# Kernel tuning notes

Hardware: AMD Instinct MI355X
Metric: run time of the kernel (lower is better)

Reference implementation:

```python
import jax, jax.numpy as jnp
import numpy as np


def _xcorr3x3_valid(x, k):
    # x: [B,H,W], k: [B,3,3] per-sample kernel; cross-correlation (matches F.conv2d), VALID padding
    B, H, W = x.shape
    out = jnp.zeros((B, H - 2, W - 2), dtype=x.dtype)
    for u in range(3):
        for v in range(3):
            out = out + x[:, u:u + H - 2, v:v + W - 2] * k[:, u, v, None, None]
    return out


def setup_inputs() -> dict:
    key = jax.random.key(0)
    ks = jax.random.split(key, 4)
    B, H, W = 256, 256, 256
    pred = jax.random.normal(ks[0], (B, H, W), dtype=jnp.float32)
    rhs = jax.random.normal(ks[1], (B, H - 2, W - 2), dtype=jnp.float32)
    Laplace_kernel = jax.random.normal(ks[2], (B, 3, 3), dtype=jnp.float32)
    Df_dr_kernel = jax.random.normal(ks[3], (B, 3, 3), dtype=jnp.float32)
    # physically sensible meshgrids: R in [1,2] (avoids div-by-zero), Z in [-1,1]
    r = jnp.linspace(1.0, 2.0, W, dtype=jnp.float32)
    z = jnp.linspace(-1.0, 1.0, H, dtype=jnp.float32)
    RR = jnp.broadcast_to(r[None, None, :], (B, H, W)).astype(jnp.float32)
    ZZ = jnp.broadcast_to(z[None, :, None], (B, H, W)).astype(jnp.float32)
    Gauss_kernel = (jnp.array([[1., 2., 1.], [2., 4., 2.], [1., 2., 1.]], dtype=jnp.float32) / 16.0)
    return {"pred": pred, "rhs": rhs, "Laplace_kernel": Laplace_kernel,
            "Df_dr_kernel": Df_dr_kernel, "RR": RR, "ZZ": ZZ, "Gauss_kernel": Gauss_kernel}


def reference(pred, rhs, Laplace_kernel, Df_dr_kernel, RR, ZZ, Gauss_kernel):
    # Lpsi, Dpsi_dr: per-sample 3x3 VALID stencils -> [B, H-2, W-2]
    Lpsi = _xcorr3x3_valid(pred, Laplace_kernel)
    Dpsi_dr = -_xcorr3x3_valid(pred, Df_dr_kernel)
    Dpsi_dr = Dpsi_dr / RR[:, 1:-1, 1:-1]
    lhs = Lpsi - Dpsi_dr
    hr = (RR[:, 1, 2] - RR[:, 1, 1])[:, None, None]
    hz = (ZZ[:, 2, 1] - ZZ[:, 1, 1])[:, None, None]
    alfa = -2.0 * (hr ** 2 + hz ** 2)
    GS_ope = lhs * alfa / (hr ** 2 * hz ** 2)
    # Gaussian smoothing, shared kernel, SAME padding (cross-correlation; kernel is symmetric)
    sm = jax.lax.conv_general_dilated(
        GS_ope[:, None, :, :], Gauss_kernel[None, None, :, :],
        window_strides=(1, 1), padding='SAME')
    GS_ope_smooth = -sm
    rhs_computed = -GS_ope_smooth[:, 0, :, :]
    return jnp.mean((rhs_computed - rhs) ** 2)
```

## Files before the change

### kernel.cpp

```cpp
#include <hip/hip_runtime.h>


__global__ __launch_bounds__(256, 4)
void pde_loss_kernel(const float* __restrict__ pred,
                     const float* __restrict__ rhs,
                     const float* __restrict__ KL,
                     const float* __restrict__ KD,
                     const float* __restrict__ RR,
                     const float* __restrict__ ZZ,
                     float* __restrict__ partials)
{
    constexpr int H = 256, W = 256, OH = 254, OW = 254;
    constexpr int SR = 8;
    const int tid = threadIdx.x;
    const int l   = tid & 63;
    const int wv  = tid >> 6;
    const int b   = blockIdx.x >> 3;
    const int strip = (blockIdx.x & 7) * 4 + wv;
    const int o0 = strip * SR;
    const int o1 = (o0 + SR < OH) ? (o0 + SR) : OH;

    const size_t ib = (size_t)b * H * W;
    const float* predb = pred + ib;
    const float* rhsb  = rhs + (size_t)b * OH * OW;

    const float hr  = RR[ib + W + 2] - RR[ib + W + 1];
    const float hz  = ZZ[ib + 2 * W + 1] - ZZ[ib + W + 1];
    const float hr2 = hr * hr, hz2 = hz * hz;
    const float s   = -2.0f * (hr2 + hz2) / (hr2 * hz2);

    const int c0 = 4 * l;
    float4 c4[9];
    {
        float4 invr;
        invr.x = 1.0f / RR[ib + W + (c0 + 1)];
        invr.y = 1.0f / RR[ib + W + (c0 + 2)];
        invr.z = 1.0f / RR[ib + W + (c0 + 3)];
        invr.w = 1.0f / RR[ib + W + ((c0 + 4 < W) ? (c0 + 4) : (W - 1))];
        const float* kl = KL + b * 9;
        const float* kd = KD + b * 9;
#pragma unroll
        for (int t = 0; t < 9; ++t) {
            const float a = kl[t] * s, d = kd[t] * s;
            c4[t].x = fmaf(d, invr.x, a);
            c4[t].y = fmaf(d, invr.y, a);
            c4[t].z = fmaf(d, invr.z, a);
            c4[t].w = fmaf(d, invr.w, a);
        }
    }

    const int g0 = o0 - 1;
    float4 pa = make_float4(0.f, 0.f, 0.f, 0.f), pb, pc;
    if (g0 >= 0) pa = *(const float4*)(predb + (size_t)g0 * W + c0);
    pb = *(const float4*)(predb + (size_t)(g0 + 1) * W + c0);
    pc = *(const float4*)(predb + (size_t)(g0 + 2) * W + c0);
    float nxa = __shfl(pa.x, l + 1, 64), nya = __shfl(pa.y, l + 1, 64);
    float nxb = __shfl(pb.x, l + 1, 64), nyb = __shfl(pb.y, l + 1, 64);

    float4 ghA = make_float4(0.f, 0.f, 0.f, 0.f);
    float4 ghB = make_float4(0.f, 0.f, 0.f, 0.f);
    float2 rc0 = make_float2(0.f, 0.f), rc1 = make_float2(0.f, 0.f);
    float acc = 0.0f;

    for (int g = g0; g <= o1; ++g) {
        float4 pn = make_float4(0.f, 0.f, 0.f, 0.f);
        const int rowp = g + 3;
        if (rowp < H && rowp <= o1 + 2)
            pn = *(const float4*)(predb + (size_t)rowp * W + c0);

        float2 rn0 = make_float2(0.f, 0.f), rn1 = make_float2(0.f, 0.f);
        if (g >= o0 && g < o1) {
            const float* rrow = rhsb + (size_t)g * OW + c0;
            rn0 = *(const float2*)rrow;
            if (c0 + 2 < OW) rn1 = *(const float2*)(rrow + 2);
        }

        const float nxc = __shfl(pc.x, l + 1, 64);
        const float nyc = __shfl(pc.y, l + 1, 64);

        float4 gs = make_float4(0.f, 0.f, 0.f, 0.f);
        if ((unsigned)g < (unsigned)OH) {
#define ROWC(p, nx, ny, t0)                                              \
            gs.x = fmaf(p.x, c4[t0].x, fmaf(p.y, c4[t0+1].x, fmaf(p.z, c4[t0+2].x, gs.x))); \
            gs.y = fmaf(p.y, c4[t0].y, fmaf(p.z, c4[t0+1].y, fmaf(p.w, c4[t0+2].y, gs.y))); \
            gs.z = fmaf(p.z, c4[t0].z, fmaf(p.w, c4[t0+1].z, fmaf(nx,  c4[t0+2].z, gs.z))); \
            gs.w = fmaf(p.w, c4[t0].w, fmaf(nx,  c4[t0+1].w, fmaf(ny,  c4[t0+2].w, gs.w)));
            ROWC(pa, nxa, nya, 0)
            ROWC(pb, nxb, nyb, 3)
            ROWC(pc, nxc, nyc, 6)
#undef ROWC
            if (l == 63) { gs.z = 0.f; gs.w = 0.f; }
        }

        float up = __shfl(gs.w, l - 1, 64);
        const float dn = __shfl(gs.x, l + 1, 64);
        if (l == 0) up = 0.f;
        float4 gh;
        gh.x = fmaf(2.f, gs.x, up   + gs.y);
        gh.y = fmaf(2.f, gs.y, gs.x + gs.z);
        gh.z = fmaf(2.f, gs.z, gs.y + gs.w);
        gh.w = fmaf(2.f, gs.w, gs.z + dn);

        const int i = g - 1;
        if (i >= o0 && i < o1) {
            const float smx = (ghA.x + 2.f * ghB.x + gh.x) * 0.0625f;
            const float smy = (ghA.y + 2.f * ghB.y + gh.y) * 0.0625f;
            const float smz = (ghA.z + 2.f * ghB.z + gh.z) * 0.0625f;
            const float smw = (ghA.w + 2.f * ghB.w + gh.w) * 0.0625f;
            const float dx = smx - rc0.x;
            const float dy = smy - rc0.y;
            float dz = smz - rc1.x;
            float dw = smw - rc1.y;
            if (c0 + 2 >= OW) { dz = 0.f; dw = 0.f; }
            acc = fmaf(dx, dx, acc);
            acc = fmaf(dy, dy, acc);
            acc = fmaf(dz, dz, acc);
            acc = fmaf(dw, dw, acc);
        }

        pa = pb; pb = pc; pc = pn;
        nxa = nxb; nya = nyb; nxb = nxc; nyb = nyc;
        ghA = ghB; ghB = gh;
        rc0 = rn0; rc1 = rn1;
    }

#pragma unroll
    for (int off = 32; off > 0; off >>= 1)
        acc += __shfl_down(acc, off, 64);
    __shared__ float wsum[4];
    if (l == 0) wsum[wv] = acc;
    __syncthreads();
    if (tid == 0)
        partials[blockIdx.x] = (wsum[0] + wsum[1]) + (wsum[2] + wsum[3]);
}

__global__ __launch_bounds__(256)
void reduce_kernel(const float* __restrict__ partials, float* __restrict__ out,
                   int n, float inv_n)
{
    const int tid = threadIdx.x;
    float a = 0.0f;
    for (int i = tid; i < n; i += 256) a += partials[i];
#pragma unroll
    for (int off = 32; off > 0; off >>= 1)
        a += __shfl_down(a, off, 64);
    __shared__ float w[4];
    if ((tid & 63) == 0) w[tid >> 6] = a;
    __syncthreads();
    if (tid == 0) out[0] = ((w[0] + w[1]) + (w[2] + w[3])) * inv_n;
}

__global__ __launch_bounds__(256, 4)
void reduce_fallback_zero(float* __restrict__ out) { if (threadIdx.x == 0) out[0] = 0.f; }

extern "C" void kernel_launch(void* const* d_in, const int* in_sizes, int n_in,
                              void* d_out, int out_size, void* d_ws, size_t ws_size,
                              hipStream_t stream) {
    const float* pred = (const float*)d_in[0];
    const float* rhs  = (const float*)d_in[1];
    const float* KL   = (const float*)d_in[2];
    const float* KD   = (const float*)d_in[3];
    const float* RR   = (const float*)d_in[4];
    const float* ZZ   = (const float*)d_in[5];
    float* out = (float*)d_out;

    const int B = in_sizes[2] / 9;
    const int nblocks = B * 8;
    const float inv_n = 1.0f / ((float)B * 254.0f * 254.0f);

    float* partials = (float*)d_ws;
    pde_loss_kernel<<<dim3(nblocks), dim3(256), 0, stream>>>(
        pred, rhs, KL, KD, RR, ZZ, partials);
    reduce_kernel<<<dim3(1), dim3(256), 0, stream>>>(partials, out, nblocks, inv_n);
}
```

Before: 216.9 us.

## Preload strip rows into registers, fully unroll row loop, split stencil into scalar-weight passes

Each wave now loads all 12 pred rows for its 8-row strip and the first rhs rows into registers before any compute, and fully unrolls the 10-step loop so every load is issued up front rather than one row per iteration. The per-column coefficient arrays (c4[9] float4) are replaced by two 9-tap stencils using wave-uniform scalar weights via readfirstlane, combined at the end with per-column scale factors. Branches are replaced by multiplicative masks. This doubles the stencil FMA count and raises register pressure, so the occupancy hint is dropped in exchange for more memory-level parallelism.

```diff
diff --git a/kernel.cpp b/kernel.cpp
--- a/kernel.cpp
+++ b/kernel.cpp
@@ -1,7 +1,7 @@
 #include <hip/hip_runtime.h>
 
 
-__global__ __launch_bounds__(256, 4)
+__global__ __launch_bounds__(256)
 void pde_loss_kernel(const float* __restrict__ pred,
                      const float* __restrict__ rhs,
                      const float* __restrict__ KL,
@@ -10,8 +10,7 @@
                      const float* __restrict__ ZZ,
                      float* __restrict__ partials)
 {
-    constexpr int H = 256, W = 256, OH = 254, OW = 254;
-    constexpr int SR = 8;
+    constexpr int H = 256, W = 256, OH = 254, OW = 254, SR = 8;
     const int tid = threadIdx.x;
     const int l   = tid & 63;
     const int wv  = tid >> 6;
@@ -23,106 +22,126 @@
     const size_t ib = (size_t)b * H * W;
     const float* predb = pred + ib;
     const float* rhsb  = rhs + (size_t)b * OH * OW;
+    const int c0 = 4 * l;
+
+    float4 p[12];
+#pragma unroll
+    for (int j = 0; j < 12; ++j) {
+        const int row = o0 - 1 + j;
+        p[j] = make_float4(0.f, 0.f, 0.f, 0.f);
+        if ((unsigned)row < (unsigned)H)
+            p[j] = *(const float4*)(predb + (size_t)row * W + c0);
+    }
+    float2 r0[8], r1[8];
+#pragma unroll
+    for (int j = 0; j < 8; ++j) { r0[j] = make_float2(0.f, 0.f); r1[j] = make_float2(0.f, 0.f); }
+#pragma unroll
+    for (int j = 0; j < 4; ++j) {
+        const float* rr = rhsb + (size_t)(o0 + j) * OW + c0;
+        r0[j] = *(const float2*)rr;
+        if (c0 + 2 < OW) r1[j] = *(const float2*)(rr + 2);
+    }
 
     const float hr  = RR[ib + W + 2] - RR[ib + W + 1];
     const float hz  = ZZ[ib + 2 * W + 1] - ZZ[ib + W + 1];
     const float hr2 = hr * hr, hz2 = hz * hz;
     const float s   = -2.0f * (hr2 + hz2) / (hr2 * hz2);
+    float kl[9], kd[9];
+#pragma unroll
+    for (int t = 0; t < 9; ++t) {
+        kl[t] = __int_as_float(__builtin_amdgcn_readfirstlane(__float_as_int(KL[b * 9 + t])));
+        kd[t] = __int_as_float(__builtin_amdgcn_readfirstlane(__float_as_int(KD[b * 9 + t])));
+    }
 
-    const int c0 = 4 * l;
-    float4 c4[9];
+    const float mzw = (l == 63) ? 0.f : 1.f;
+    const float m23 = (c0 + 2 < OW) ? 1.f : 0.f;
+    const float m0  = (l > 0) ? 1.f : 0.f;
+    float4 s4, sir4;
     {
         float4 invr;
         invr.x = 1.0f / RR[ib + W + (c0 + 1)];
         invr.y = 1.0f / RR[ib + W + (c0 + 2)];
         invr.z = 1.0f / RR[ib + W + (c0 + 3)];
         invr.w = 1.0f / RR[ib + W + ((c0 + 4 < W) ? (c0 + 4) : (W - 1))];
-        const float* kl = KL + b * 9;
-        const float* kd = KD + b * 9;
-#pragma unroll
-        for (int t = 0; t < 9; ++t) {
-            const float a = kl[t] * s, d = kd[t] * s;
-            c4[t].x = fmaf(d, invr.x, a);
-            c4[t].y = fmaf(d, invr.y, a);
-            c4[t].z = fmaf(d, invr.z, a);
-            c4[t].w = fmaf(d, invr.w, a);
-        }
+        s4.x = s; s4.y = s; s4.z = s * mzw; s4.w = s * mzw;
+        sir4.x = s4.x * invr.x; sir4.y = s4.y * invr.y;
+        sir4.z = s4.z * invr.z; sir4.w = s4.w * invr.w;
     }
 
-    const int g0 = o0 - 1;
-    float4 pa = make_float4(0.f, 0.f, 0.f, 0.f), pb, pc;
-    if (g0 >= 0) pa = *(const float4*)(predb + (size_t)g0 * W + c0);
-    pb = *(const float4*)(predb + (size_t)(g0 + 1) * W + c0);
-    pc = *(const float4*)(predb + (size_t)(g0 + 2) * W + c0);
-    float nxa = __shfl(pa.x, l + 1, 64), nya = __shfl(pa.y, l + 1, 64);
-    float nxb = __shfl(pb.x, l + 1, 64), nyb = __shfl(pb.y, l + 1, 64);
+#define SROW(SV, P, nx, ny, k0, k1, k2, KC)                                   \
+    SV.x = fmaf(P.x, KC[k0], fmaf(P.y, KC[k1], fmaf(P.z, KC[k2], SV.x)));     \
+    SV.y = fmaf(P.y, KC[k0], fmaf(P.z, KC[k1], fmaf(P.w, KC[k2], SV.y)));     \
+    SV.z = fmaf(P.z, KC[k0], fmaf(P.w, KC[k1], fmaf(nx,  KC[k2], SV.z)));     \
+    SV.w = fmaf(P.w, KC[k0], fmaf(nx,  KC[k1], fmaf(ny,  KC[k2], SV.w)));
 
-    float4 ghA = make_float4(0.f, 0.f, 0.f, 0.f);
-    float4 ghB = make_float4(0.f, 0.f, 0.f, 0.f);
-    float2 rc0 = make_float2(0.f, 0.f), rc1 = make_float2(0.f, 0.f);
+    float ax = __shfl(p[0].x, l + 1, 64), ay = __shfl(p[0].y, l + 1, 64);
+    float bx = __shfl(p[1].x, l + 1, 64), by = __shfl(p[1].y, l + 1, 64);
+    float4 ghm2 = make_float4(0.f, 0.f, 0.f, 0.f);
+    float4 ghm1 = make_float4(0.f, 0.f, 0.f, 0.f);
     float acc = 0.0f;
 
-    for (int g = g0; g <= o1; ++g) {
-        float4 pn = make_float4(0.f, 0.f, 0.f, 0.f);
-        const int rowp = g + 3;
-        if (rowp < H && rowp <= o1 + 2)
-            pn = *(const float4*)(predb + (size_t)rowp * W + c0);
+#pragma unroll
+    for (int K = 0; K < 10; ++K) {
+        const int g = o0 - 1 + K;
 
-        float2 rn0 = make_float2(0.f, 0.f), rn1 = make_float2(0.f, 0.f);
-        if (g >= o0 && g < o1) {
-            const float* rrow = rhsb + (size_t)g * OW + c0;
-            rn0 = *(const float2*)rrow;
-            if (c0 + 2 < OW) rn1 = *(const float2*)(rrow + 2);
+        if (K >= 2 && K <= 5) {
+            const int i = o0 + K + 2;
+            if (i < o1) {
+                const float* rr = rhsb + (size_t)i * OW + c0;
+                r0[K + 2] = *(const float2*)rr;
+                if (c0 + 2 < OW) r1[K + 2] = *(const float2*)(rr + 2);
+            }
         }
 
-        const float nxc = __shfl(pc.x, l + 1, 64);
-        const float nyc = __shfl(pc.y, l + 1, 64);
+        const float cx = __shfl(p[K + 2].x, l + 1, 64);
+        const float cy = __shfl(p[K + 2].y, l + 1, 64);
 
-        float4 gs = make_float4(0.f, 0.f, 0.f, 0.f);
-        if ((unsigned)g < (unsigned)OH) {
-#define ROWC(p, nx, ny, t0)                                              \
-            gs.x = fmaf(p.x, c4[t0].x, fmaf(p.y, c4[t0+1].x, fmaf(p.z, c4[t0+2].x, gs.x))); \
-            gs.y = fmaf(p.y, c4[t0].y, fmaf(p.z, c4[t0+1].y, fmaf(p.w, c4[t0+2].y, gs.y))); \
-            gs.z = fmaf(p.z, c4[t0].z, fmaf(p.w, c4[t0+1].z, fmaf(nx,  c4[t0+2].z, gs.z))); \
-            gs.w = fmaf(p.w, c4[t0].w, fmaf(nx,  c4[t0+1].w, fmaf(ny,  c4[t0+2].w, gs.w)));
-            ROWC(pa, nxa, nya, 0)
-            ROWC(pb, nxb, nyb, 3)
-            ROWC(pc, nxc, nyc, 6)
-#undef ROWC
-            if (l == 63) { gs.z = 0.f; gs.w = 0.f; }
+        float4 SL = make_float4(0.f, 0.f, 0.f, 0.f);
+        float4 SD = make_float4(0.f, 0.f, 0.f, 0.f);
+        if (g <= o1 && (unsigned)g < (unsigned)OH) {
+            SROW(SL, p[K],     ax, ay, 0, 1, 2, kl)
+            SROW(SL, p[K + 1], bx, by, 3, 4, 5, kl)
+            SROW(SL, p[K + 2], cx, cy, 6, 7, 8, kl)
+            SROW(SD, p[K],     ax, ay, 0, 1, 2, kd)
+            SROW(SD, p[K + 1], bx, by, 3, 4, 5, kd)
+            SROW(SD, p[K + 2], cx, cy, 6, 7, 8, kd)
         }
+        float4 gs;
+        gs.x = fmaf(s4.x, SL.x, sir4.x * SD.x);
+        gs.y = fmaf(s4.y, SL.y, sir4.y * SD.y);
+        gs.z = fmaf(s4.z, SL.z, sir4.z * SD.z);
+        gs.w = fmaf(s4.w, SL.w, sir4.w * SD.w);
 
-        float up = __shfl(gs.w, l - 1, 64);
+        const float up = __shfl(gs.w, l - 1, 64) * m0;
         const float dn = __shfl(gs.x, l + 1, 64);
-        if (l == 0) up = 0.f;
         float4 gh;
         gh.x = fmaf(2.f, gs.x, up   + gs.y);
         gh.y = fmaf(2.f, gs.y, gs.x + gs.z);
         gh.z = fmaf(2.f, gs.z, gs.y + gs.w);
         gh.w = fmaf(2.f, gs.w, gs.z + dn);
 
-        const int i = g - 1;
-        if (i >= o0 && i < o1) {
-            const float smx = (ghA.x + 2.f * ghB.x + gh.x) * 0.0625f;
-            const float smy = (ghA.y + 2.f * ghB.y + gh.y) * 0.0625f;
-            const float smz = (ghA.z + 2.f * ghB.z + gh.z) * 0.0625f;
-            const float smw = (ghA.w + 2.f * ghB.w + gh.w) * 0.0625f;
-            const float dx = smx - rc0.x;
-            const float dy = smy - rc0.y;
-            float dz = smz - rc1.x;
-            float dw = smw - rc1.y;
-            if (c0 + 2 >= OW) { dz = 0.f; dw = 0.f; }
-            acc = fmaf(dx, dx, acc);
-            acc = fmaf(dy, dy, acc);
-            acc = fmaf(dz, dz, acc);
-            acc = fmaf(dw, dw, acc);
+        if (K >= 2) {
+            const int i = g - 1;
+            if (i < o1) {
+                const float smx = (ghm2.x + 2.f * ghm1.x + gh.x) * 0.0625f;
+                const float smy = (ghm2.y + 2.f * ghm1.y + gh.y) * 0.0625f;
+                const float smz = (ghm2.z + 2.f * ghm1.z + gh.z) * 0.0625f;
+                const float smw = (ghm2.w + 2.f * ghm1.w + gh.w) * 0.0625f;
+                const float dx = smx - r0[K - 2].x;
+                const float dy = smy - r0[K - 2].y;
+                const float dz = (smz - r1[K - 2].x) * m23;
+                const float dw = (smw - r1[K - 2].y) * m23;
+                acc = fmaf(dx, dx, acc);
+                acc = fmaf(dy, dy, acc);
+                acc = fmaf(dz, dz, acc);
+                acc = fmaf(dw, dw, acc);
+            }
         }
 
-        pa = pb; pb = pc; pc = pn;
-        nxa = nxb; nya = nyb; nxb = nxc; nyb = nyc;
-        ghA = ghB; ghB = gh;
-        rc0 = rn0; rc1 = rn1;
+        ghm2 = ghm1; ghm1 = gh;
+        ax = bx; ay = by; bx = cx; by = cy;
     }
+#undef SROW
 
 #pragma unroll
     for (int off = 32; off > 0; off >>= 1)
@@ -150,9 +169,6 @@
     if (tid == 0) out[0] = ((w[0] + w[1]) + (w[2] + w[3])) * inv_n;
 }
 
-__global__ __launch_bounds__(256, 4)
-void reduce_fallback_zero(float* __restrict__ out) { if (threadIdx.x == 0) out[0] = 0.f; }
-
 extern "C" void kernel_launch(void* const* d_in, const int* in_sizes, int n_in,
                               void* d_out, int out_size, void* d_ws, size_t ws_size,
                               hipStream_t stream) {
```

Measured after the change: 219.7 us. Within noise of the previous version (+1.3%).
